# Kernel tuning notes

Measured on AMD Instinct MI355X. Metric: run time of the kernel, lower is better.

Reference implementation:

```python
import jax, jax.numpy as jnp
import numpy as np

SEQ = 2048          # prompt length (x.size(0) > 1 path)
D_IN = 4096         # weight.size(1)
N_OUT = 11008       # weight.size(0), Llama-7B FFN width
SPARSITY = 0.4      # fraction of neurons kept globally
TOKEN_SPARSITY = 0.2  # per-token top-k fraction (common.get_core_neurons)


def setup_inputs() -> dict:
    key = jax.random.key(0)
    kx, kw, kb = jax.random.split(key, 3)
    x = jax.random.normal(kx, (SEQ, D_IN), dtype=jnp.float16)
    weight = jax.random.normal(kw, (N_OUT, D_IN), dtype=jnp.float16) * jnp.float16(0.02)
    bias = jax.random.normal(kb, (N_OUT,), dtype=jnp.float16) * jnp.float16(0.02)
    return {"x": x, "weight": weight, "bias": bias}


def get_core_neurons(true_value, token_sparsity, sparsity, n_neurons):
    # Per-token top-k activations -> count how often each neuron appears ->
    # keep the globally most frequent `sparsity * n_neurons` neurons (sorted).
    k_tok = int(token_sparsity * n_neurons)
    remained = int(sparsity * n_neurons)
    _, tok_idx = jax.lax.top_k(true_value.astype(jnp.float32), k_tok)  # [SEQ, k_tok]
    counts = jnp.zeros((n_neurons,), dtype=jnp.int32).at[tok_idx.reshape(-1)].add(1)
    _, core_idx = jax.lax.top_k(counts, remained)
    return jnp.sort(core_idx)


def reference(x, weight, bias):
    # Prompt path: full GEMM in fp16, then core-neuron selection + weight gather.
    true_value = x @ weight.T + bias                      # [SEQ, N_OUT] fp16
    core_idx = get_core_neurons(true_value, TOKEN_SPARSITY, SPARSITY, weight.shape[0])
    filtered_W = weight[core_idx, :]                      # [remained, D_IN]
    filtered_bias = bias[core_idx]                        # [remained]
    return true_value, filtered_W, filtered_bias
```

## Files before the change

kernel.cpp:

```cpp
#include <hip/hip_runtime.h>

typedef __attribute__((ext_vector_type(8))) _Float16 half8;
typedef __attribute__((ext_vector_type(4))) float floatx4;
typedef unsigned short us_t;

#define SEQ   2048
#define DIN   4096
#define NOUT  11008
#define KTOK  2201
#define NCORE 4403
#define NCHUNK 43
#define NT2   512
#define NCH2  22
#define NBLK  1376

__device__ __forceinline__ unsigned pk2(float a, float b) {
  auto h = __builtin_amdgcn_cvt_pkrtz(a, b);
  return __builtin_bit_cast(unsigned, h);
}
__device__ __forceinline__ unsigned fkey32(unsigned u) {
  return u ^ ((u >> 31) ? 0xFFFFFFFFu : 0x80000000u);
}
__device__ __forceinline__ void gl2lds16(const us_t* g, us_t* l) {
  __builtin_amdgcn_global_load_lds(
      (const __attribute__((address_space(1))) unsigned int*)(g),
      (__attribute__((address_space(3))) unsigned int*)(l), 16, 0, 0);
}

__device__ __forceinline__ int wave_suffix_incl(int x, int lane) {
#pragma unroll
  for (int off = 1; off < 64; off <<= 1) {
    int y = __shfl_down(x, off);
    x += (lane + off < 64) ? y : 0;
  }
  return x;
}

template <int G, int NW>
__device__ __forceinline__ void find_thr(const int* hist, int above, int K,
                                         int* wtot, int* shv,
                                         int t, int lane, int wv) {
  int val = 0;
#pragma unroll
  for (int j = 0; j < G; ++j) val += hist[t * G + j];
  int x = wave_suffix_incl(val, lane);
  if (lane == 0) wtot[wv] = x;
  __syncthreads();
  int add = 0;
#pragma unroll
  for (int w2 = 0; w2 < NW; ++w2) add += (w2 > wv) ? wtot[w2] : 0;
  const int suf = x + add;
  const int sufn = suf - val;
  if (above + suf >= K && above + sufn < K) {
    int cum = above + sufn;
    for (int v = t * G + G - 1; v >= t * G; --v) {
      if (cum + hist[v] >= K) { shv[0] = v; shv[1] = cum; break; }
      cum += hist[v];
    }
  }
  __syncthreads();
}

__global__ __launch_bounds__(256) void cvt_f16(const float* __restrict__ src,
                                               unsigned* __restrict__ dst, int n8) {
  int i = blockIdx.x * 256 + threadIdx.x;
  if (i >= n8) return;
  const float4* s = (const float4*)src + (size_t)i * 2;
  float4 a = s[0], b = s[1];
  uint4 o = {pk2(a.x, a.y), pk2(a.z, a.w), pk2(b.x, b.y), pk2(b.z, b.w)};
  ((uint4*)dst)[i] = o;
}

__global__ __launch_bounds__(256) void gemm_f16(const us_t* __restrict__ X16,
                                                const us_t* __restrict__ W16,
                                                const float* __restrict__ Bias,
                                                float* __restrict__ C) {
  __shared__ __attribute__((aligned(16))) us_t As[128 * 32];
  __shared__ __attribute__((aligned(16))) us_t Bs[128 * 32];
  const int t = threadIdx.x;

  const int id = blockIdx.x;
  const int wg = ((id & 7) * (NBLK / 8)) + (id >> 3);
  const int n0 = (wg >> 4) * 128;
  const int m0 = (wg & 15) * 128;

  const int l = t & 63, w = t >> 6;
  const int r = l & 15, q = l >> 4;
  const int wm = (w >> 1) * 64, wn = (w & 1) * 64;

  const us_t* Ag = X16 + (size_t)(m0 + (t >> 2)) * DIN + (t & 3) * 8;
  const us_t* Bg = W16 + (size_t)(n0 + (t >> 2)) * DIN + (t & 3) * 8;
  us_t* la = As + t * 8;
  us_t* lb = Bs + t * 8;

  floatx4 acc[4][4] = {};
  const us_t* pa = As + (wm + r) * 32 + q * 8;
  const us_t* pb = Bs + (wn + r) * 32 + q * 8;

  for (int kt = 0; kt < DIN; kt += 32) {
    gl2lds16(Ag + kt, la);
    gl2lds16(Ag + kt + 64 * DIN, la + 2048);
    gl2lds16(Bg + kt, lb);
    gl2lds16(Bg + kt + 64 * DIN, lb + 2048);
    __syncthreads();
    half8 af[4];
#pragma unroll
    for (int im = 0; im < 4; ++im)
      af[im] = *(const half8*)(pa + im * 16 * 32);
#pragma unroll
    for (int in = 0; in < 4; ++in) {
      half8 bfv = *(const half8*)(pb + in * 16 * 32);
#pragma unroll
      for (int im = 0; im < 4; ++im)
        acc[im][in] = __builtin_amdgcn_mfma_f32_16x16x32_f16(af[im], bfv, acc[im][in], 0, 0, 0);
    }
    __syncthreads();
  }
#pragma unroll
  for (int in = 0; in < 4; ++in) {
    const int col = n0 + wn + in * 16 + r;
    const float bv = Bias[col];
#pragma unroll
    for (int im = 0; im < 4; ++im) {
      const int row = m0 + wm + im * 16 + q * 4;
#pragma unroll
      for (int i = 0; i < 4; ++i)
        C[(size_t)(row + i) * NOUT + col] = acc[im][in][i] + bv;
    }
  }
}

__global__ __launch_bounds__(256) void gemm_bias(const float* __restrict__ X,
                                                 const float* __restrict__ W,
                                                 const float* __restrict__ Bias,
                                                 float* __restrict__ C) {
  __shared__ __attribute__((aligned(16))) us_t As[128 * 32];
  __shared__ __attribute__((aligned(16))) us_t Bs[128 * 32];
  const int t = threadIdx.x;
  const int m0 = blockIdx.y * 128, n0 = blockIdx.x * 128;
  const int l = t & 63, w = t >> 6;
  const int r = l & 15, q = l >> 4;
  const int wm = (w >> 1) * 64, wn = (w & 1) * 64;
  const float* Ag = X + (size_t)(m0 + (t >> 2)) * DIN + (t & 3) * 8;
  const float* Bg = W + (size_t)(n0 + (t >> 2)) * DIN + (t & 3) * 8;
  us_t* la = As + t * 8;
  us_t* lb = Bs + t * 8;
  floatx4 acc[4][4] = {};
  const us_t* pa = As + (wm + r) * 32 + q * 8;
  const us_t* pb = Bs + (wn + r) * 32 + q * 8;
  for (int kt = 0; kt < DIN; kt += 32) {
    float4 a0 = *(const float4*)(Ag + kt);
    float4 a1 = *(const float4*)(Ag + kt + 4);
    float4 a2 = *(const float4*)(Ag + kt + 64 * DIN);
    float4 a3 = *(const float4*)(Ag + kt + 64 * DIN + 4);
    float4 b0 = *(const float4*)(Bg + kt);
    float4 b1 = *(const float4*)(Bg + kt + 4);
    float4 b2 = *(const float4*)(Bg + kt + 64 * DIN);
    float4 b3 = *(const float4*)(Bg + kt + 64 * DIN + 4);
    uint4 ua  = {pk2(a0.x, a0.y), pk2(a0.z, a0.w), pk2(a1.x, a1.y), pk2(a1.z, a1.w)};
    uint4 ua2 = {pk2(a2.x, a2.y), pk2(a2.z, a2.w), pk2(a3.x, a3.y), pk2(a3.z, a3.w)};
    uint4 ub  = {pk2(b0.x, b0.y), pk2(b0.z, b0.w), pk2(b1.x, b1.y), pk2(b1.z, b1.w)};
    uint4 ub2 = {pk2(b2.x, b2.y), pk2(b2.z, b2.w), pk2(b3.x, b3.y), pk2(b3.z, b3.w)};
    *(uint4*)la = ua;
    *(uint4*)(la + 2048) = ua2;
    *(uint4*)lb = ub;
    *(uint4*)(lb + 2048) = ub2;
    __syncthreads();
    half8 af[4];
#pragma unroll
    for (int im = 0; im < 4; ++im)
      af[im] = *(const half8*)(pa + im * 16 * 32);
#pragma unroll
    for (int in = 0; in < 4; ++in) {
      half8 bfv = *(const half8*)(pb + in * 16 * 32);
#pragma unroll
      for (int im = 0; im < 4; ++im)
        acc[im][in] = __builtin_amdgcn_mfma_f32_16x16x32_f16(af[im], bfv, acc[im][in], 0, 0, 0);
    }
    __syncthreads();
  }
#pragma unroll
  for (int in = 0; in < 4; ++in) {
    const int col = n0 + wn + in * 16 + r;
    const float bv = Bias[col];
#pragma unroll
    for (int im = 0; im < 4; ++im) {
      const int row = m0 + wm + im * 16 + q * 4;
#pragma unroll
      for (int i = 0; i < 4; ++i)
        C[(size_t)(row + i) * NOUT + col] = acc[im][in][i] + bv;
    }
  }
}

__global__ __launch_bounds__(NT2) void row_topk(const float* __restrict__ TV,
                                                int* __restrict__ counts) {
  __shared__ __attribute__((aligned(16))) unsigned keys[NOUT];
  __shared__ int hist[2048];
  __shared__ int wtot[NT2 / 64];
  __shared__ int shv[2];
  __shared__ int cnte[NCH2 * (NT2 / 64)];
  const int t = threadIdx.x;
  const int lane = t & 63, wv = t >> 6;

  for (int i = t; i < 2048; i += NT2) hist[i] = 0;
  __syncthreads();
  const uint4* src = (const uint4*)(TV + (size_t)blockIdx.x * NOUT);
  for (int i = t; i < NOUT / 4; i += NT2) {
    uint4 v = src[i];
    unsigned k0 = fkey32(v.x), k1 = fkey32(v.y), k2 = fkey32(v.z), k3 = fkey32(v.w);
    uint4 kk = {k0, k1, k2, k3};
    *(uint4*)&keys[i * 4] = kk;
    atomicAdd(&hist[k0 >> 21], 1);
    atomicAdd(&hist[k1 >> 21], 1);
    atomicAdd(&hist[k2 >> 21], 1);
    atomicAdd(&hist[k3 >> 21], 1);
  }
  __syncthreads();
  find_thr<4, NT2 / 64>(hist, 0, KTOK, wtot, shv, t, lane, wv);
  const unsigned b1 = (unsigned)shv[0];
  const int above1 = shv[1];
  __syncthreads();

  for (int i = t; i < 2048; i += NT2) hist[i] = 0;
  __syncthreads();
  for (int i = t; i < NOUT; i += NT2) {
    unsigned k = keys[i];
    if ((k >> 21) == b1) atomicAdd(&hist[(k >> 10) & 0x7FF], 1);
  }
  __syncthreads();
  find_thr<4, NT2 / 64>(hist, above1, KTOK, wtot, shv, t, lane, wv);
  const unsigned b2 = (unsigned)shv[0];
  const int above2 = shv[1];
  const unsigned pref2 = (b1 << 11) | b2;
  __syncthreads();

  for (int i = t; i < 1024; i += NT2) hist[i] = 0;
  __syncthreads();
  for (int i = t; i < NOUT; i += NT2) {
    unsigned k = keys[i];
    if ((k >> 10) == pref2) atomicAdd(&hist[k & 0x3FF], 1);
  }
  __syncthreads();
  find_thr<2, NT2 / 64>(hist, above2, KTOK, wtot, shv, t, lane, wv);
  const unsigned T = (pref2 << 10) | (unsigned)shv[0];
  const int need = KTOK - shv[1];

  for (int c = 0; c < NCH2; ++c) {
    const int i = c * NT2 + t;
    const bool valid = i < NOUT;
    const unsigned k = valid ? keys[i] : 0u;
    if (valid && k > T) atomicAdd(&counts[i], 1);
    unsigned long long me = __ballot(valid && (k == T));
    if (lane == 0) cnte[c * (NT2 / 64) + wv] = __popcll(me);
  }
  __syncthreads();
  for (int c = 0; c < NCH2; ++c) {
    const int i = c * NT2 + t;
    const bool valid = i < NOUT;
    const unsigned k = valid ? keys[i] : 0u;
    const bool eq = valid && (k == T);
    unsigned long long me = __ballot(eq);
    if (eq) {
      int rank = __popcll(me & ((1ULL << lane) - 1));
      const int idx = c * (NT2 / 64) + wv;
      for (int j = 0; j < idx; ++j) rank += cnte[j];
      if (rank < need) atomicAdd(&counts[i], 1);
    }
  }
}

__global__ __launch_bounds__(256) void select_core(const int* __restrict__ counts,
                                                   const float* __restrict__ Bias,
                                                   int* __restrict__ core_idx,
                                                   float* __restrict__ bias_out) {
  __shared__ int cl[NOUT];
  __shared__ int hist[2049];
  __shared__ int wtot[4];
  __shared__ int shv[2];
  __shared__ int tabS[256];
  const int t = threadIdx.x;
  const int lane = t & 63, wv = t >> 6;
  for (int i = t; i < NOUT; i += 256) cl[i] = counts[i];
  for (int i = t; i < 2049; i += 256) hist[i] = 0;
  __syncthreads();
  for (int i = t; i < NOUT; i += 256) atomicAdd(&hist[cl[i]], 1);
  __syncthreads();
  {
    int val = 0;
#pragma unroll
    for (int j = 0; j < 8; ++j) val += hist[t * 8 + j];
    if (t == 255) val += hist[2048];
    int x = wave_suffix_incl(val, lane);
    if (lane == 0) wtot[wv] = x;
    __syncthreads();
    int add = 0;
#pragma unroll
    for (int w2 = 0; w2 < 4; ++w2) add += (w2 > wv) ? wtot[w2] : 0;
    const int suf = x + add;
    const int sufn = suf - val;
    if (suf >= NCORE && sufn < NCORE) {
      int cum = sufn;
      const int hi = (t == 255) ? 2048 : t * 8 + 7;
      for (int v = hi; v >= t * 8; --v) {
        if (cum + hist[v] >= NCORE) { shv[0] = v; shv[1] = NCORE - cum; break; }
        cum += hist[v];
      }
    }
    __syncthreads();
  }
  const int Cv = shv[0], need2 = shv[1];
  for (int c = 0; c < NCHUNK; ++c) {
    const int i = c * 256 + t;
    const int cnt = cl[i];
    unsigned long long mg = __ballot(cnt > Cv);
    unsigned long long me = __ballot(cnt == Cv);
    if (lane == 0) tabS[c * 4 + wv] = __popcll(mg) | (__popcll(me) << 16);
    else if (c == 0) tabS[c * 4 + wv] = tabS[c * 4 + wv];
  }
  if (t >= NCHUNK * 4) tabS[t] = 0;
  __syncthreads();
  {
    const int orig = tabS[t];
    int x = orig;
#pragma unroll
    for (int off = 1; off < 64; off <<= 1) {
      int y = __shfl_up(x, off);
      x += (lane >= off) ? y : 0;
    }
    if (lane == 63) wtot[wv] = x;
    __syncthreads();
    int add = 0;
#pragma unroll
    for (int w2 = 0; w2 < 4; ++w2) add += (w2 < wv) ? wtot[w2] : 0;
    const int excl = x - orig + add;
    __syncthreads();
    tabS[t] = excl;
    __syncthreads();
  }
  const unsigned long long lm = (1ULL << lane) - 1;
  for (int c = 0; c < NCHUNK; ++c) {
    const int i = c * 256 + t;
    const int cnt = cl[i];
    const bool g = cnt > Cv, e = cnt == Cv;
    unsigned long long mg = __ballot(g);
    unsigned long long me = __ballot(e);
    const int P = tabS[c * 4 + wv];
    const int gpre = (P & 0xFFFF) + __popcll(mg & lm);
    const int epre = (P >> 16) + __popcll(me & lm);
    const bool sel = g || (e && epre < need2);
    if (sel) {
      const int pos = gpre + (epre < need2 ? epre : need2);
      core_idx[pos] = i;
      bias_out[pos] = Bias[i];
    }
  }
}

__global__ __launch_bounds__(256) void gather_rows16(const us_t* __restrict__ W16,
                                                     const int* __restrict__ core_idx,
                                                     float* __restrict__ outW) {
  const int b = blockIdx.x;
  const int j = core_idx[b];
  const half8* src = (const half8*)(W16 + (size_t)j * DIN);
  float4* dst = (float4*)(outW + (size_t)b * DIN);
  for (int i = threadIdx.x; i < DIN / 8; i += 256) {
    half8 h = src[i];
    float4 lo = {(float)h[0], (float)h[1], (float)h[2], (float)h[3]};
    float4 hi = {(float)h[4], (float)h[5], (float)h[6], (float)h[7]};
    dst[i * 2] = lo;
    dst[i * 2 + 1] = hi;
  }
}

__global__ __launch_bounds__(256) void gather_rows(const float* __restrict__ W,
                                                   const int* __restrict__ core_idx,
                                                   float* __restrict__ outW) {
  const int b = blockIdx.x;
  const int j = core_idx[b];
  const float4* src = (const float4*)(W + (size_t)j * DIN);
  float4* dst = (float4*)(outW + (size_t)b * DIN);
  for (int i = threadIdx.x; i < DIN / 4; i += 256) dst[i] = src[i];
}

__global__ __launch_bounds__(256) void zero_counts(int* __restrict__ counts) {
  counts[blockIdx.x * 256 + threadIdx.x] = 0;
}

extern "C" void kernel_launch(void* const* d_in, const int* in_sizes, int n_in,
                              void* d_out, int out_size, void* d_ws, size_t ws_size,
                              hipStream_t stream) {
  const float* X    = (const float*)d_in[0];
  const float* W    = (const float*)d_in[1];
  const float* Bias = (const float*)d_in[2];
  float* out_tv = (float*)d_out;
  float* out_w  = out_tv + (size_t)SEQ * NOUT;
  float* out_b  = out_w + (size_t)NCORE * DIN;
  int* counts   = (int*)d_ws;
  int* core_idx = counts + NOUT;

  const size_t meta = 64 * 1024;
  const size_t need_ws = meta + ((size_t)SEQ * DIN + (size_t)NOUT * DIN) * sizeof(us_t);

  zero_counts<<<NOUT / 256, 256, 0, stream>>>(counts);
  if (ws_size >= need_ws) {
    us_t* X16 = (us_t*)((char*)d_ws + meta);
    us_t* W16 = X16 + (size_t)SEQ * DIN;
    cvt_f16<<<(SEQ * DIN / 8 + 255) / 256, 256, 0, stream>>>(X, (unsigned*)X16, SEQ * DIN / 8);
    cvt_f16<<<(NOUT * DIN / 8 + 255) / 256, 256, 0, stream>>>(W, (unsigned*)W16, NOUT * DIN / 8);
    gemm_f16<<<NBLK, 256, 0, stream>>>(X16, W16, Bias, out_tv);
    row_topk<<<SEQ, NT2, 0, stream>>>(out_tv, counts);
    select_core<<<1, 256, 0, stream>>>(counts, Bias, core_idx, out_b);
    gather_rows16<<<NCORE, 256, 0, stream>>>(W16, core_idx, out_w);
  } else {
    gemm_bias<<<dim3(NOUT / 128, SEQ / 128), 256, 0, stream>>>(X, W, Bias, out_tv);
    row_topk<<<SEQ, NT2, 0, stream>>>(out_tv, counts);
    select_core<<<1, 256, 0, stream>>>(counts, Bias, core_idx, out_b);
    gather_rows<<<NCORE, 256, 0, stream>>>(W, core_idx, out_w);
  }
}
```

Before: 681.7 us.

## Replace global atomic counts with per-row selection bitmaps and a column popcount pass

The per-row top-k kernel now writes a 64-bit selection bitmap per wave chunk, reusing the freed X16 buffer, instead of issuing global atomicAdds into a shared counts array. A new count_bits kernel then sums the bits column-wise across all rows to produce the neuron counts, which also removes the zero_counts launch on this path. This is meant to avoid heavy global atomic contention on 11008 counters from 2048 blocks. The cost is an extra launch and a strided read of a bitmap of about 2.8 MB.

```diff
diff --git a/kernel.cpp b/kernel.cpp
--- a/kernel.cpp
+++ b/kernel.cpp
@@ -12,6 +12,7 @@
 #define NCHUNK 43
 #define NT2   512
 #define NCH2  22
+#define NWRD  172
 #define NBLK  1376
 
 __device__ __forceinline__ unsigned pk2(float a, float b) {
@@ -193,8 +194,8 @@
   }
 }
 
-__global__ __launch_bounds__(NT2) void row_topk(const float* __restrict__ TV,
-                                                int* __restrict__ counts) {
+__global__ __launch_bounds__(NT2) void row_topk_bm(const float* __restrict__ TV,
+                                                   unsigned long long* __restrict__ bitmap) {
   __shared__ __attribute__((aligned(16))) unsigned keys[NOUT];
   __shared__ int hist[2048];
   __shared__ int wtot[NT2 / 64];
@@ -235,6 +236,106 @@
   const unsigned pref2 = (b1 << 11) | b2;
   __syncthreads();
 
+  for (int i = t; i < 1024; i += NT2) hist[i] = 0;
+  __syncthreads();
+  for (int i = t; i < NOUT; i += NT2) {
+    unsigned k = keys[i];
+    if ((k >> 10) == pref2) atomicAdd(&hist[k & 0x3FF], 1);
+  }
+  __syncthreads();
+  find_thr<2, NT2 / 64>(hist, above2, KTOK, wtot, shv, t, lane, wv);
+  const unsigned T = (pref2 << 10) | (unsigned)shv[0];
+  const int need = KTOK - shv[1];
+
+  for (int c = 0; c < NCH2; ++c) {
+    const int i = c * NT2 + t;
+    const bool valid = i < NOUT;
+    const unsigned k = valid ? keys[i] : 0u;
+    unsigned long long me = __ballot(valid && (k == T));
+    if (lane == 0) cnte[c * (NT2 / 64) + wv] = __popcll(me);
+  }
+  __syncthreads();
+  unsigned long long* dst = bitmap + (size_t)blockIdx.x * NWRD;
+  for (int c = 0; c < NCH2; ++c) {
+    const int i = c * NT2 + t;
+    const bool valid = i < NOUT;
+    const unsigned k = valid ? keys[i] : 0u;
+    const bool eq = valid && (k == T);
+    bool sel = valid && (k > T);
+    unsigned long long me = __ballot(eq);
+    if (eq) {
+      int rank = __popcll(me & ((1ULL << lane) - 1));
+      const int idx = c * (NT2 / 64) + wv;
+      for (int j = 0; j < idx; ++j) rank += cnte[j];
+      sel = sel || (rank < need);
+    }
+    unsigned long long mask = __ballot(sel);
+    const int wrd = c * (NT2 / 64) + wv;
+    if (lane == 0 && wrd < NWRD) dst[wrd] = mask;
+  }
+}
+
+__global__ __launch_bounds__(256) void count_bits(const unsigned long long* __restrict__ bm,
+                                                  int* __restrict__ counts) {
+  __shared__ int part[4][64];
+  const int t = threadIdx.x, lane = t & 63, wv = t >> 6;
+  const int wrd = blockIdx.x;
+  const unsigned long long* p = bm + wrd;
+  int cnt = 0;
+  const int r0 = wv * (SEQ / 4);
+  for (int r = r0; r < r0 + SEQ / 4; r += 8) {
+#pragma unroll
+    for (int j = 0; j < 8; ++j) {
+      unsigned long long v = p[(size_t)(r + j) * NWRD];
+      cnt += (int)((v >> lane) & 1ULL);
+    }
+  }
+  part[wv][lane] = cnt;
+  __syncthreads();
+  if (wv == 0)
+    counts[wrd * 64 + lane] = part[0][lane] + part[1][lane] + part[2][lane] + part[3][lane];
+}
+
+__global__ __launch_bounds__(NT2) void row_topk(const float* __restrict__ TV,
+                                                int* __restrict__ counts) {
+  __shared__ __attribute__((aligned(16))) unsigned keys[NOUT];
+  __shared__ int hist[2048];
+  __shared__ int wtot[NT2 / 64];
+  __shared__ int shv[2];
+  __shared__ int cnte[NCH2 * (NT2 / 64)];
+  const int t = threadIdx.x;
+  const int lane = t & 63, wv = t >> 6;
+
+  for (int i = t; i < 2048; i += NT2) hist[i] = 0;
+  __syncthreads();
+  const uint4* src = (const uint4*)(TV + (size_t)blockIdx.x * NOUT);
+  for (int i = t; i < NOUT / 4; i += NT2) {
+    uint4 v = src[i];
+    unsigned k0 = fkey32(v.x), k1 = fkey32(v.y), k2 = fkey32(v.z), k3 = fkey32(v.w);
+    uint4 kk = {k0, k1, k2, k3};
+    *(uint4*)&keys[i * 4] = kk;
+    atomicAdd(&hist[k0 >> 21], 1);
+    atomicAdd(&hist[k1 >> 21], 1);
+    atomicAdd(&hist[k2 >> 21], 1);
+    atomicAdd(&hist[k3 >> 21], 1);
+  }
+  __syncthreads();
+  find_thr<4, NT2 / 64>(hist, 0, KTOK, wtot, shv, t, lane, wv);
+  const unsigned b1 = (unsigned)shv[0];
+  const int above1 = shv[1];
+  __syncthreads();
+  for (int i = t; i < 2048; i += NT2) hist[i] = 0;
+  __syncthreads();
+  for (int i = t; i < NOUT; i += NT2) {
+    unsigned k = keys[i];
+    if ((k >> 21) == b1) atomicAdd(&hist[(k >> 10) & 0x7FF], 1);
+  }
+  __syncthreads();
+  find_thr<4, NT2 / 64>(hist, above1, KTOK, wtot, shv, t, lane, wv);
+  const unsigned b2 = (unsigned)shv[0];
+  const int above2 = shv[1];
+  const unsigned pref2 = (b1 << 11) | b2;
+  __syncthreads();
   for (int i = t; i < 1024; i += NT2) hist[i] = 0;
   __syncthreads();
   for (int i = t; i < NOUT; i += NT2) {
@@ -316,7 +417,6 @@
     unsigned long long mg = __ballot(cnt > Cv);
     unsigned long long me = __ballot(cnt == Cv);
     if (lane == 0) tabS[c * 4 + wv] = __popcll(mg) | (__popcll(me) << 16);
-    else if (c == 0) tabS[c * 4 + wv] = tabS[c * 4 + wv];
   }
   if (t >= NCHUNK * 4) tabS[t] = 0;
   __syncthreads();
@@ -402,17 +502,19 @@
   const size_t meta = 64 * 1024;
   const size_t need_ws = meta + ((size_t)SEQ * DIN + (size_t)NOUT * DIN) * sizeof(us_t);
 
-  zero_counts<<<NOUT / 256, 256, 0, stream>>>(counts);
   if (ws_size >= need_ws) {
     us_t* X16 = (us_t*)((char*)d_ws + meta);
     us_t* W16 = X16 + (size_t)SEQ * DIN;
+    unsigned long long* bitmap = (unsigned long long*)X16;
     cvt_f16<<<(SEQ * DIN / 8 + 255) / 256, 256, 0, stream>>>(X, (unsigned*)X16, SEQ * DIN / 8);
     cvt_f16<<<(NOUT * DIN / 8 + 255) / 256, 256, 0, stream>>>(W, (unsigned*)W16, NOUT * DIN / 8);
     gemm_f16<<<NBLK, 256, 0, stream>>>(X16, W16, Bias, out_tv);
-    row_topk<<<SEQ, NT2, 0, stream>>>(out_tv, counts);
+    row_topk_bm<<<SEQ, NT2, 0, stream>>>(out_tv, bitmap);
+    count_bits<<<NWRD, 256, 0, stream>>>(bitmap, counts);
     select_core<<<1, 256, 0, stream>>>(counts, Bias, core_idx, out_b);
     gather_rows16<<<NCORE, 256, 0, stream>>>(W16, core_idx, out_w);
   } else {
+    zero_counts<<<NOUT / 256, 256, 0, stream>>>(counts);
     gemm_bias<<<dim3(NOUT / 128, SEQ / 128), 256, 0, stream>>>(X, W, Bias, out_tv);
     row_topk<<<SEQ, NT2, 0, stream>>>(out_tv, counts);
     select_core<<<1, 256, 0, stream>>>(counts, Bias, core_idx, out_b);
```

Result: no change. 685.4 us (+0.5%).
